# Optimization experiments

Hardware: AMD Instinct MI355X
Metric: run time of the kernel (lower is better)

The kernel has to match this reference:

```python
import jax, jax.numpy as jnp
import numpy as np

N = 50000   # nodes
E = 800000  # edges per relation (avg degree 16)
IN = 128    # input feature dim
H = 2       # attention heads per layer
OUT = 64    # output feats per head
R = 2       # number of relations
NEG_SLOPE = 0.2


def _edge_softmax(e, dst, n):
    # e: [E, H] edge scores; softmax over incoming edges of each dst node
    m = jax.ops.segment_max(e, dst, num_segments=n)  # [N, H]
    m = jnp.where(jnp.isfinite(m), m, 0.0)
    ex = jnp.exp(e - jax.lax.stop_gradient(m)[dst])
    s = jax.ops.segment_sum(ex, dst, num_segments=n)  # [N, H]
    return ex / s[dst]


def _gat_layer(h, W, al, ar, b, src, dst):
    # h: [N, in]; W: [R, in, H*OUT]; al/ar: [R, H, OUT]; b: [R, H*OUT]
    # src/dst: [R, E] int32. HeteroGraphConv with sum aggregation over relations.
    acc = jnp.zeros((N, H, OUT), h.dtype)
    for r in range(R):  # small fixed relation count
        f = (h @ W[r]).reshape(N, H, OUT)           # projected feats
        el = (f * al[r]).sum(-1)                    # [N, H]
        er = (f * ar[r]).sum(-1)                    # [N, H]
        e = jax.nn.leaky_relu(el[src[r]] + er[dst[r]], NEG_SLOPE)  # [E, H]
        a = _edge_softmax(e, dst[r], N)             # [E, H]
        msg = f[src[r]] * a[:, :, None]             # [E, H, OUT]
        agg = jax.ops.segment_sum(msg, dst[r], num_segments=N)     # [N, H, OUT]
        acc = acc + jax.nn.elu(agg + b[r].reshape(1, H, OUT))
    return acc.reshape(N, H * OUT)  # flatten(1)


def setup_inputs() -> dict:
    key = jax.random.key(0)
    k = jax.random.split(key, 13)
    s = 0.05
    f32 = jnp.float32
    return {
        "x": jax.random.normal(k[0], (N, IN), f32),
        "W0": jax.random.normal(k[1], (R, IN, H * OUT), f32) * s,
        "al0": jax.random.normal(k[2], (R, H, OUT), f32) * s,
        "ar0": jax.random.normal(k[3], (R, H, OUT), f32) * s,
        "b0": jax.random.normal(k[4], (R, H * OUT), f32) * s,
        "W1": jax.random.normal(k[5], (R, H * OUT, H * OUT), f32) * s,
        "al1": jax.random.normal(k[6], (R, H, OUT), f32) * s,
        "ar1": jax.random.normal(k[7], (R, H, OUT), f32) * s,
        "b1": jax.random.normal(k[8], (R, H * OUT), f32) * s,
        "src0": jax.random.randint(k[9], (R, E), 0, N, jnp.int32),
        "dst0": jax.random.randint(k[10], (R, E), 0, N, jnp.int32),
        "src1": jax.random.randint(k[11], (R, E), 0, N, jnp.int32),
        "dst1": jax.random.randint(k[12], (R, E), 0, N, jnp.int32),
    }


def reference(x, W0, al0, ar0, b0, W1, al1, ar1, b1, src0, dst0, src1, dst1):
    h = _gat_layer(x, W0, al0, ar0, b0, src0, dst0)  # [N, H*OUT]
    h = _gat_layer(h, W1, al1, ar1, b1, src1, dst1)  # [N, H*OUT]
    return h
```

## Files before the change

### kernel.cpp

```cpp
#include <hip/hip_runtime.h>

#define NN 50000
#define NE 800000
#define DIM 128
#define NB 128
#define CH 4096
#define CAP 8192

typedef unsigned int uint;
typedef unsigned short ushort;
typedef __attribute__((ext_vector_type(8))) short v8s;
typedef __attribute__((ext_vector_type(4))) float v4f;

__device__ __forceinline__ ushort f2bf(float f) {
    union { float f; uint i; } c; c.f = f;
    const uint r = (c.i + 0x7fffu + ((c.i >> 16) & 1u)) >> 16;
    return (ushort)r;
}

__global__ __launch_bounds__(256) void conv_wt(
    const float* __restrict__ W0, const float* __restrict__ W1,
    ushort* __restrict__ WT)
{
    const int t = blockIdx.x * 256 + threadIdx.x;
#pragma unroll
    for (int i = 0; i < 4; i++) {
        const int o = t * 4 + i;
        const int m = o >> 14, rem = o & 16383;
        const int nrow = rem >> 7, k = rem & 127;
        const float* src = (m < 2) ? (W0 + (size_t)m * 16384)
                                   : (W1 + (size_t)(m - 2) * 16384);
        WT[o] = f2bf(src[k * 128 + nrow]);
    }
}

__global__ __launch_bounds__(256) void gemm_dual(
    const ushort* __restrict__ hbf, const float* __restrict__ xf,
    const ushort* __restrict__ WT,
    const float* __restrict__ al, const float* __restrict__ ar,
    ushort* __restrict__ fg0, ushort* __restrict__ fg1,
    float* __restrict__ elb, int n, int is_f32)
{
    __shared__ ushort tile[64][136];
    const int tid = threadIdx.x;
    const int w = tid >> 6, lane = tid & 63;
    const int quad = lane >> 4, l16 = lane & 15;
    const int row0 = blockIdx.x * 64 + w * 16;

    int arow = row0 + l16;
    if (arow >= n) arow = n - 1;

    v8s afr[4];
    if (is_f32) {
        const float* ap = xf + (size_t)arow * DIM + quad * 8;
#pragma unroll
        for (int kt = 0; kt < 4; kt++) {
            const float4 a0 = *(const float4*)(ap + kt * 32);
            const float4 a1 = *(const float4*)(ap + kt * 32 + 4);
            ushort tmp[8] = { f2bf(a0.x), f2bf(a0.y), f2bf(a0.z), f2bf(a0.w),
                              f2bf(a1.x), f2bf(a1.y), f2bf(a1.z), f2bf(a1.w) };
            afr[kt] = *(const v8s*)tmp;
        }
    } else {
        const ushort* ap = hbf + (size_t)arow * DIM + quad * 8;
#pragma unroll
        for (int kt = 0; kt < 4; kt++) afr[kt] = *(const v8s*)(ap + kt * 32);
    }

    for (int rel = 0; rel < 2; rel++) {
        const ushort* bp = WT + (size_t)rel * DIM * DIM + (size_t)l16 * DIM + quad * 8;
        v4f acc[8];
#pragma unroll
        for (int nt = 0; nt < 8; nt++) acc[nt] = (v4f)0.0f;
#pragma unroll
        for (int kt = 0; kt < 4; kt++) {
#pragma unroll
            for (int nt = 0; nt < 8; nt++) {
                const v8s b = *(const v8s*)(bp + (size_t)nt * 16 * DIM + kt * 32);
                acc[nt] = __builtin_amdgcn_mfma_f32_16x16x32_bf16(afr[kt], b, acc[nt], 0, 0, 0);
            }
        }

        const float* alr = al + rel * DIM;
        const float* arr = ar + rel * DIM;
        float pel[4][2], per2[4][2];
#pragma unroll
        for (int r = 0; r < 4; r++)
            pel[r][0] = pel[r][1] = per2[r][0] = per2[r][1] = 0.f;
#pragma unroll
        for (int nt = 0; nt < 8; nt++) {
            const int col = nt * 16 + l16;
            const float av = alr[col], rv = arr[col];
            const int head = nt >> 2;
#pragma unroll
            for (int r = 0; r < 4; r++) {
                pel[r][head] += acc[nt][r] * av;
                per2[r][head] += acc[nt][r] * rv;
            }
        }
#pragma unroll
        for (int o = 1; o < 16; o <<= 1) {
#pragma unroll
            for (int r = 0; r < 4; r++) {
#pragma unroll
                for (int h = 0; h < 2; h++) {
                    pel[r][h] += __shfl_xor(pel[r][h], o);
                    per2[r][h] += __shfl_xor(per2[r][h], o);
                }
            }
        }
        float* elp = elb + (size_t)rel * NN * 4;
        float* erp = elp + (size_t)NN * 2;
        if (l16 == 0) {
#pragma unroll
            for (int r = 0; r < 4; r++) {
                const int row = row0 + quad * 4 + r;
                if (row < n) {
#pragma unroll
                    for (int h = 0; h < 2; h++) {
                        elp[row * 2 + h] = pel[r][h];
                        erp[row * 2 + h] = per2[r][h];
                    }
                }
            }
        }

        __syncthreads();
        const int lr0 = w * 16 + quad * 4;
#pragma unroll
        for (int nt = 0; nt < 8; nt++) {
            const int col = nt * 16 + l16;
#pragma unroll
            for (int r = 0; r < 4; r++)
                tile[lr0 + r][col] = f2bf(acc[nt][r]);
        }
        __syncthreads();
        ushort* fgr = rel ? fg1 : fg0;
        const int srow = tid >> 2, ch = tid & 3;
        const int grow = blockIdx.x * 64 + srow;
        if (grow < n) {
            const uint4* lp = (const uint4*)&tile[srow][ch * 32];
            uint4* gp = (uint4*)(fgr + (size_t)grow * DIM + ch * 32);
            gp[0] = lp[0];
            gp[1] = lp[1];
            gp[2] = lp[2];
            gp[3] = lp[3];
        }
    }
}

__global__ __launch_bounds__(512) void init_gcur(int* __restrict__ gcur)
{
    const int i = threadIdx.x;
    gcur[i] = i * CAP;
}

__global__ __launch_bounds__(256) void bin_edges(
    const int* __restrict__ dst0, const int* __restrict__ dst1,
    const int* __restrict__ src0, const int* __restrict__ src1,
    int* __restrict__ gcur, uint* __restrict__ binned)
{
    __shared__ int hist[NB], ebase[NB], lcur[NB], gbase[NB], sc[NB];
    __shared__ uint stage[CH];
    const int bpset = (NE + CH - 1) / CH;
    const int bid = blockIdx.x;
    const int s = bid / bpset, cb = bid - s * bpset;
    const int* dstp = (s < 2) ? (dst0 + (size_t)s * NE) : (dst1 + (size_t)(s - 2) * NE);
    const int* srcp = (s < 2) ? (src0 + (size_t)s * NE) : (src1 + (size_t)(s - 2) * NE);
    const int e0 = cb * CH;
    const int t = threadIdx.x;

    if (t < NB) hist[t] = 0;
    __syncthreads();

    int myd[16], mys[16];
#pragma unroll
    for (int k = 0; k < 16; k++) {
        const int e = e0 + t + k * 256;
        if (e < NE) {
            const int d = dstp[e];
            myd[k] = d;
            mys[k] = srcp[e];
            atomicAdd(&hist[(d * NB) / NN], 1);
        } else myd[k] = -1;
    }
    __syncthreads();
    if (t < NB) sc[t] = hist[t];
    __syncthreads();
    for (int o = 1; o < NB; o <<= 1) {
        int tv = 0;
        if (t < NB && t >= o) tv = sc[t - o];
        __syncthreads();
        if (t < NB) sc[t] += tv;
        __syncthreads();
    }
    if (t < NB) {
        ebase[t] = sc[t] - hist[t];
        lcur[t]  = sc[t] - hist[t];
        gbase[t] = atomicAdd(&gcur[s * NB + t], hist[t]);
    }
    __syncthreads();
#pragma unroll
    for (int k = 0; k < 16; k++) {
        if (myd[k] >= 0) {
            const int b = (myd[k] * NB) / NN;
            const int p = atomicAdd(&lcur[b], 1);
            stage[p] = ((uint)myd[k] << 16) | (uint)mys[k];
        }
    }
    __syncthreads();
    const int total = ebase[NB - 1] + hist[NB - 1];
    for (int i = t; i < total; i += 256) {
        const uint v = stage[i];
        const int b = ((int)(v >> 16) * NB) / NN;
        binned[gbase[b] + (i - ebase[b])] = v;
    }
}

__global__ __launch_bounds__(64) void scan_buckets(
    const int* __restrict__ gcur, int* __restrict__ bbase, int* __restrict__ row)
{
    const int s = threadIdx.x;
    if (s < 4) {
        int acc = 0;
        for (int b = 0; b < NB; b++) {
            bbase[s * (NB + 1) + b] = acc;
            acc += gcur[s * NB + b] - (s * NB + b) * CAP;
        }
        bbase[s * (NB + 1) + NB] = acc;
        row[s * (NN + 1) + NN] = NE;
    }
}

__global__ __launch_bounds__(256) void build_csr(
    const int* __restrict__ bbase, const uint* __restrict__ binned,
    int* __restrict__ row, ushort* __restrict__ csr_src)
{
    __shared__ int A[512], B[512], lcur[512];
    const int bid = blockIdx.x;
    const int s = bid >> 7, b = bid & (NB - 1);
    const int nb0 = (b * NN + NB - 1) / NB;
    int nb1 = ((b + 1) * NN + NB - 1) / NB;
    if (nb1 > NN) nb1 = NN;
    const int nloc = nb1 - nb0;
    const int jb = bbase[s * (NB + 1) + b], je = bbase[s * (NB + 1) + b + 1];
    const int cnt = je - jb;
    const uint* bslot = binned + (size_t)(s * NB + b) * CAP;
    const int t = threadIdx.x;

    A[t] = 0; A[t + 256] = 0;
    __syncthreads();
    for (int j = t; j < cnt; j += 256)
        atomicAdd(&A[(int)(bslot[j] >> 16) - nb0], 1);
    __syncthreads();
    const int c0 = A[t], c1 = A[t + 256];
    int* cur = A; int* nxt = B;
    for (int off = 1; off < 512; off <<= 1) {
        nxt[t]       = cur[t]       + ((t >= off)       ? cur[t - off]       : 0);
        nxt[t + 256] = cur[t + 256] + ((t + 256 >= off) ? cur[t + 256 - off] : 0);
        __syncthreads();
        int* tmp = cur; cur = nxt; nxt = tmp;
    }
    if (t < nloc) {
        const int v = jb + cur[t] - c0;
        lcur[t] = v;
        row[s * (NN + 1) + nb0 + t] = v;
    }
    if (t + 256 < nloc) {
        const int v = jb + cur[t + 256] - c1;
        lcur[t + 256] = v;
        row[s * (NN + 1) + nb0 + t + 256] = v;
    }
    __syncthreads();
    ushort* outp = csr_src + (size_t)s * NE;
    for (int j = t; j < cnt; j += 256) {
        const uint v = bslot[j];
        const int p = atomicAdd(&lcur[(int)(v >> 16) - nb0], 1);
        outp[p] = (ushort)(v & 0xffffu);
    }
}

__device__ __forceinline__ float elu(float v) { return v > 0.f ? v : expm1f(v); }
__device__ __forceinline__ float2 bfpair(uint u) {
    union { uint i; float f; } lo, hi;
    lo.i = u << 16;
    hi.i = u & 0xffff0000u;
    return make_float2(lo.f, hi.f);
}

__global__ __launch_bounds__(256) void aggregate_dual(
    const int* __restrict__ row0, const ushort* __restrict__ csr0,
    const int* __restrict__ row1, const ushort* __restrict__ csr1,
    const float2* __restrict__ el0, const float2* __restrict__ er0,
    const float2* __restrict__ el1, const float2* __restrict__ er1,
    const ushort* __restrict__ fg0, const ushort* __restrict__ fg1,
    const float* __restrict__ bias0, const float* __restrict__ bias1,
    float* __restrict__ outf, ushort* __restrict__ outbf, int obf)
{
    __shared__ uint soff[4][64];
    __shared__ float wts[4][2][64];
    const int wv = (blockIdx.x * 256 + threadIdx.x) >> 6;
    if (wv >= NN) return;
    const int lane = threadIdx.x & 63;
    const int wid = threadIdx.x >> 6;

    const int* rows[2] = {row0, row1};
    const ushort* csrs[2] = {csr0, csr1};
    const float2* els[2] = {el0, el1};
    const float2* ers[2] = {er0, er1};
    const ushort* fgs[2] = {fg0, fg1};
    const float* biases[2] = {bias0, bias1};

    float oacc0 = 0.f, oacc1 = 0.f;

#pragma unroll
    for (int rel = 0; rel < 2; rel++) {
        const int beg = rows[rel][wv], end = rows[rel][wv + 1];
        const int deg = end - beg;
        const float2 erd = ers[rel][wv];
        float2 acc = make_float2(0.f, 0.f);

        if (deg <= 64) {
            uint sof = 0;
            float ex0 = 0.f, ex1 = 0.f;
            if (lane < deg) {
                const int s = csrs[rel][beg + lane];
                const float2 e = els[rel][s];
                float e0 = e.x + erd.x, e1 = e.y + erd.y;
                e0 = e0 > 0.f ? e0 : 0.2f * e0;
                e1 = e1 > 0.f ? e1 : 0.2f * e1;
                ex0 = __expf(e0);
                ex1 = __expf(e1);
                sof = (uint)s << 8;
            }
            float den0 = ex0, den1 = ex1;
            for (int o = 32; o > 0; o >>= 1) {
                den0 += __shfl_xor(den0, o);
                den1 += __shfl_xor(den1, o);
            }
            const float inv0 = 1.0f / den0, inv1 = 1.0f / den1;
            soff[wid][lane] = sof;
            wts[wid][0][lane] = ex0 * inv0;
            wts[wid][1][lane] = ex1 * inv1;
            const char* fgb = (const char*)fgs[rel] + lane * 4;
            const float* wrow = wts[wid][lane >> 5];
            const uint* sorow = soff[wid];
            const int dp = (deg + 15) & ~15;
            for (int tt = 0; tt < dp; tt += 16) {
                uint off[16];
                float wgt[16];
#pragma unroll
                for (int k = 0; k < 16; k++) {
                    off[k] = sorow[tt + k];
                    wgt[k] = wrow[tt + k];
                }
                uint u[16];
#pragma unroll
                for (int k = 0; k < 16; k++)
                    u[k] = *(const uint*)(fgb + off[k]);
#pragma unroll
                for (int k = 0; k < 16; k++) {
                    const float2 f = bfpair(u[k]);
                    acc.x += f.x * wgt[k];
                    acc.y += f.y * wgt[k];
                }
            }
        } else {
            float den0 = 0.f, den1 = 0.f;
            for (int c0 = beg; c0 < end; c0 += 64) {
                const int j = c0 + lane;
                if (j < end) {
                    const float2 e = els[rel][csrs[rel][j]];
                    float e0 = e.x + erd.x, e1 = e.y + erd.y;
                    e0 = e0 > 0.f ? e0 : 0.2f * e0;
                    e1 = e1 > 0.f ? e1 : 0.2f * e1;
                    den0 += __expf(e0);
                    den1 += __expf(e1);
                }
            }
            for (int o = 32; o > 0; o >>= 1) {
                den0 += __shfl_xor(den0, o);
                den1 += __shfl_xor(den1, o);
            }
            const float inv0 = 1.0f / den0, inv1 = 1.0f / den1;
            for (int c0 = beg; c0 < end; c0 += 64) {
                const int j = c0 + lane;
                int s = -1;
                float ex0 = 0.f, ex1 = 0.f;
                if (j < end) {
                    s = csrs[rel][j];
                    const float2 e = els[rel][s];
                    float e0 = e.x + erd.x, e1 = e.y + erd.y;
                    e0 = e0 > 0.f ? e0 : 0.2f * e0;
                    e1 = e1 > 0.f ? e1 : 0.2f * e1;
                    ex0 = __expf(e0) * inv0;
                    ex1 = __expf(e1) * inv1;
                }
                const int cm = min(64, end - c0);
                for (int tt = 0; tt < cm; tt++) {
                    const int st = __shfl(s, tt);
                    const float a0 = __shfl(ex0, tt);
                    const float a1 = __shfl(ex1, tt);
                    const float aa = (lane < 32) ? a0 : a1;
                    const float2 fv = bfpair(
                        *(const uint*)((const char*)fgs[rel] + ((size_t)st << 8) + lane * 4));
                    acc.x += fv.x * aa;
                    acc.y += fv.y * aa;
                }
            }
        }

        const float b0 = biases[rel][2 * lane], b1 = biases[rel][2 * lane + 1];
        oacc0 += elu(acc.x + b0);
        oacc1 += elu(acc.y + b1);
    }

    if (obf) {
        ushort tmp[2] = { f2bf(oacc0), f2bf(oacc1) };
        *(uint*)(outbf + (size_t)wv * DIM + 2 * lane) = *(const uint*)tmp;
    } else {
        float* op = outf + (size_t)wv * DIM + 2 * lane;
        op[0] = oacc0; op[1] = oacc1;
    }
}

extern "C" void kernel_launch(void* const* d_in, const int* in_sizes, int n_in,
                              void* d_out, int out_size, void* d_ws, size_t ws_size,
                              hipStream_t stream)
{
    const float* x   = (const float*)d_in[0];
    const float* W0  = (const float*)d_in[1];
    const float* al0 = (const float*)d_in[2];
    const float* ar0 = (const float*)d_in[3];
    const float* b0  = (const float*)d_in[4];
    const float* W1  = (const float*)d_in[5];
    const float* al1 = (const float*)d_in[6];
    const float* ar1 = (const float*)d_in[7];
    const float* b1  = (const float*)d_in[8];
    const int* src0 = (const int*)d_in[9];
    const int* dst0 = (const int*)d_in[10];
    const int* src1 = (const int*)d_in[11];
    const int* dst1 = (const int*)d_in[12];
    float* out = (float*)d_out;

    char* w = (char*)d_ws;
    auto alloc = [&](size_t bytes) {
        char* p = w; w += (bytes + 255) & ~(size_t)255; return p;
    };
    ushort* h1bf   = (ushort*)alloc((size_t)NN * DIM * 2);
    ushort* fg0    = (ushort*)alloc((size_t)NN * DIM * 2);
    ushort* fg1    = (ushort*)alloc((size_t)NN * DIM * 2);
    ushort* WT     = (ushort*)alloc((size_t)4 * DIM * DIM * 2);
    float*  elb    = (float*)alloc((size_t)8 * NN * 4);
    int*    row    = (int*)alloc((size_t)4 * (NN + 1) * 4);
    ushort* csr    = (ushort*)alloc((size_t)4 * NE * 2);
    uint*   binned = (uint*)alloc((size_t)4 * NB * CAP * 4);
    int*    bbase  = (int*)alloc((size_t)4 * (NB + 1) * 4);
    int*    gcur   = (int*)alloc((size_t)4 * NB * 4);

    conv_wt<<<64, 256, 0, stream>>>(W0, W1, WT);
    init_gcur<<<1, 512, 0, stream>>>(gcur);
    {
        const int bpset = (NE + CH - 1) / CH;
        bin_edges<<<4 * bpset, 256, 0, stream>>>(dst0, dst1, src0, src1, gcur, binned);
    }
    scan_buckets<<<1, 64, 0, stream>>>(gcur, bbase, row);
    build_csr<<<4 * NB, 256, 0, stream>>>(bbase, binned, row, csr);

    const int gblocks = (NN + 63) / 64;
    for (int L = 0; L < 2; L++) {
        const ushort* WTl = WT + (size_t)L * 2 * DIM * DIM;
        const float* al  = L ? al1 : al0;
        const float* ar  = L ? ar1 : ar0;
        const float* b   = L ? b1 : b0;
        gemm_dual<<<gblocks, 256, 0, stream>>>(
            L ? h1bf : nullptr, L ? nullptr : x, WTl, al, ar,
            fg0, fg1, elb, NN, L ? 0 : 1);
        const int es0 = L * 2, es1 = L * 2 + 1;
        float* el0p = elb;
        float* er0p = elb + (size_t)NN * 2;
        float* el1p = elb + (size_t)NN * 4;
        float* er1p = elb + (size_t)NN * 6;
        aggregate_dual<<<(NN * 64 + 255) / 256, 256, 0, stream>>>(
            row + es0 * (NN + 1), csr + (size_t)es0 * NE,
            row + es1 * (NN + 1), csr + (size_t)es1 * NE,
            (const float2*)el0p, (const float2*)er0p,
            (const float2*)el1p, (const float2*)er1p,
            fg0, fg1, b, b + DIM,
            L ? out : nullptr, L ? nullptr : h1bf, L ? 0 : 1);
    }
}
```

Before: 355.0 us.

## Interleave both relations' gathers in aggregate, fuse gcur init, parallelize bucket scan

```diff
diff --git a/kernel.cpp b/kernel.cpp
--- a/kernel.cpp
+++ b/kernel.cpp
@@ -20,8 +20,14 @@
 
 __global__ __launch_bounds__(256) void conv_wt(
     const float* __restrict__ W0, const float* __restrict__ W1,
-    ushort* __restrict__ WT)
-{
+    ushort* __restrict__ WT, int* __restrict__ gcur)
+{
+    if (blockIdx.x == 64) {
+        const int t = threadIdx.x;
+        gcur[t] = t * CAP;
+        gcur[t + 256] = (t + 256) * CAP;
+        return;
+    }
     const int t = blockIdx.x * 256 + threadIdx.x;
 #pragma unroll
     for (int i = 0; i < 4; i++) {
@@ -149,12 +155,6 @@
     }
 }
 
-__global__ __launch_bounds__(512) void init_gcur(int* __restrict__ gcur)
-{
-    const int i = threadIdx.x;
-    gcur[i] = i * CAP;
-}
-
 __global__ __launch_bounds__(256) void bin_edges(
     const int* __restrict__ dst0, const int* __restrict__ dst1,
     const int* __restrict__ src0, const int* __restrict__ src1,
@@ -217,17 +217,24 @@
     }
 }
 
-__global__ __launch_bounds__(64) void scan_buckets(
+__global__ __launch_bounds__(512) void scan_buckets(
     const int* __restrict__ gcur, int* __restrict__ bbase, int* __restrict__ row)
 {
-    const int s = threadIdx.x;
-    if (s < 4) {
-        int acc = 0;
-        for (int b = 0; b < NB; b++) {
-            bbase[s * (NB + 1) + b] = acc;
-            acc += gcur[s * NB + b] - (s * NB + b) * CAP;
-        }
-        bbase[s * (NB + 1) + NB] = acc;
+    __shared__ int sc[512];
+    const int t = threadIdx.x;
+    const int s = t >> 7, b = t & (NB - 1);
+    const int cnt = gcur[t] - t * CAP;
+    sc[t] = cnt;
+    __syncthreads();
+    for (int o = 1; o < NB; o <<= 1) {
+        const int add = (b >= o) ? sc[t - o] : 0;
+        __syncthreads();
+        sc[t] += add;
+        __syncthreads();
+    }
+    bbase[s * (NB + 1) + b] = sc[t] - cnt;
+    if (b == NB - 1) {
+        bbase[s * (NB + 1) + NB] = sc[t];
         row[s * (NN + 1) + NN] = NE;
     }
 }
@@ -297,8 +304,8 @@
     const float* __restrict__ bias0, const float* __restrict__ bias1,
     float* __restrict__ outf, ushort* __restrict__ outbf, int obf)
 {
-    __shared__ uint soff[4][64];
-    __shared__ float wts[4][2][64];
+    __shared__ uint soff[4][2][64];
+    __shared__ float wts[4][2][2][64];
     const int wv = (blockIdx.x * 256 + threadIdx.x) >> 6;
     if (wv >= NN) return;
     const int lane = threadIdx.x & 63;
@@ -313,18 +320,20 @@
 
     float oacc0 = 0.f, oacc1 = 0.f;
 
-#pragma unroll
-    for (int rel = 0; rel < 2; rel++) {
-        const int beg = rows[rel][wv], end = rows[rel][wv + 1];
-        const int deg = end - beg;
-        const float2 erd = ers[rel][wv];
-        float2 acc = make_float2(0.f, 0.f);
-
-        if (deg <= 64) {
+    const int beg0 = rows[0][wv], d0 = rows[0][wv + 1] - beg0;
+    const int beg1 = rows[1][wv], d1 = rows[1][wv + 1] - beg1;
+
+    if (d0 <= 64 && d1 <= 64) {
+        const int begs[2] = {beg0, beg1};
+        const int degs[2] = {d0, d1};
+#pragma unroll
+        for (int rel = 0; rel < 2; rel++) {
+            const int deg = degs[rel];
+            const float2 erd = ers[rel][wv];
             uint sof = 0;
             float ex0 = 0.f, ex1 = 0.f;
             if (lane < deg) {
-                const int s = csrs[rel][beg + lane];
+                const int s = csrs[rel][begs[rel] + lane];
                 const float2 e = els[rel][s];
                 float e0 = e.x + erd.x, e1 = e.y + erd.y;
                 e0 = e0 > 0.f ? e0 : 0.2f * e0;
@@ -339,33 +348,72 @@
                 den1 += __shfl_xor(den1, o);
             }
             const float inv0 = 1.0f / den0, inv1 = 1.0f / den1;
-            soff[wid][lane] = sof;
-            wts[wid][0][lane] = ex0 * inv0;
-            wts[wid][1][lane] = ex1 * inv1;
-            const char* fgb = (const char*)fgs[rel] + lane * 4;
-            const float* wrow = wts[wid][lane >> 5];
-            const uint* sorow = soff[wid];
-            const int dp = (deg + 15) & ~15;
-            for (int tt = 0; tt < dp; tt += 16) {
-                uint off[16];
-                float wgt[16];
+            soff[wid][rel][lane] = sof;
+            wts[wid][rel][0][lane] = ex0 * inv0;
+            wts[wid][rel][1][lane] = ex1 * inv1;
+        }
+
+        const char* fgb0 = (const char*)fgs[0] + lane * 4;
+        const char* fgb1 = (const char*)fgs[1] + lane * 4;
+        const uint* so0 = soff[wid][0];
+        const uint* so1 = soff[wid][1];
+        const float* w0row = wts[wid][0][lane >> 5];
+        const float* w1row = wts[wid][1][lane >> 5];
+        const int dp0 = (d0 + 15) & ~15;
+        const int dp1 = (d1 + 15) & ~15;
+        const int dpm = dp0 > dp1 ? dp0 : dp1;
+        float2 acc0 = make_float2(0.f, 0.f), acc1 = make_float2(0.f, 0.f);
+
+        for (int tt = 0; tt < dpm; tt += 16) {
+            const bool go0 = tt < dp0, go1 = tt < dp1;
+            uint off0[16], off1[16];
+            uint u0[16], u1[16];
+            if (go0) {
+#pragma unroll
+                for (int k = 0; k < 16; k++) off0[k] = so0[tt + k];
+            }
+            if (go1) {
+#pragma unroll
+                for (int k = 0; k < 16; k++) off1[k] = so1[tt + k];
+            }
+            if (go0) {
+#pragma unroll
+                for (int k = 0; k < 16; k++)
+                    u0[k] = *(const uint*)(fgb0 + off0[k]);
+            }
+            if (go1) {
+#pragma unroll
+                for (int k = 0; k < 16; k++)
+                    u1[k] = *(const uint*)(fgb1 + off1[k]);
+            }
+            if (go0) {
 #pragma unroll
                 for (int k = 0; k < 16; k++) {
-                    off[k] = sorow[tt + k];
-                    wgt[k] = wrow[tt + k];
-                }
-                uint u[16];
-#pragma unroll
-                for (int k = 0; k < 16; k++)
-                    u[k] = *(const uint*)(fgb + off[k]);
+                    const float2 f = bfpair(u0[k]);
+                    const float wg = w0row[tt + k];
+                    acc0.x += f.x * wg;
+                    acc0.y += f.y * wg;
+                }
+            }
+            if (go1) {
 #pragma unroll
                 for (int k = 0; k < 16; k++) {
-                    const float2 f = bfpair(u[k]);
-                    acc.x += f.x * wgt[k];
-                    acc.y += f.y * wgt[k];
-                }
-            }
-        } else {
+                    const float2 f = bfpair(u1[k]);
+                    const float wg = w1row[tt + k];
+                    acc1.x += f.x * wg;
+                    acc1.y += f.y * wg;
+                }
+            }
+        }
+
+        oacc0 = elu(acc0.x + biases[0][2 * lane]) + elu(acc1.x + biases[1][2 * lane]);
+        oacc1 = elu(acc0.y + biases[0][2 * lane + 1]) + elu(acc1.y + biases[1][2 * lane + 1]);
+    } else {
+#pragma unroll
+        for (int rel = 0; rel < 2; rel++) {
+            const int beg = rows[rel][wv], end = rows[rel][wv + 1];
+            const float2 erd = ers[rel][wv];
+            float2 acc = make_float2(0.f, 0.f);
             float den0 = 0.f, den1 = 0.f;
             for (int c0 = beg; c0 < end; c0 += 64) {
                 const int j = c0 + lane;
@@ -408,11 +456,10 @@
                     acc.y += fv.y * aa;
                 }
             }
-        }
-
-        const float b0 = biases[rel][2 * lane], b1 = biases[rel][2 * lane + 1];
-        oacc0 += elu(acc.x + b0);
-        oacc1 += elu(acc.y + b1);
+            const float b0 = biases[rel][2 * lane], b1 = biases[rel][2 * lane + 1];
+            oacc0 += elu(acc.x + b0);
+            oacc1 += elu(acc.y + b1);
+        }
     }
 
     if (obf) {
@@ -458,13 +505,12 @@
     int*    bbase  = (int*)alloc((size_t)4 * (NB + 1) * 4);
     int*    gcur   = (int*)alloc((size_t)4 * NB * 4);
 
-    conv_wt<<<64, 256, 0, stream>>>(W0, W1, WT);
-    init_gcur<<<1, 512, 0, stream>>>(gcur);
+    conv_wt<<<65, 256, 0, stream>>>(W0, W1, WT, gcur);
     {
         const int bpset = (NE + CH - 1) / CH;
         bin_edges<<<4 * bpset, 256, 0, stream>>>(dst0, dst1, src0, src1, gcur, binned);
     }
-    scan_buckets<<<1, 64, 0, stream>>>(gcur, bbase, row);
+    scan_buckets<<<1, 512, 0, stream>>>(gcur, bbase, row);
     build_csr<<<4 * NB, 256, 0, stream>>>(bbase, binned, row, csr);
 
     const int gblocks = (NN + 63) / 64;
```

Result: slower. 403.2 us (+13.6%).
